# Optimization experiments

Measured on AMD Instinct MI355X. Metric: run time of the kernel, lower is better.

The kernel has to match this reference:

```python
import jax, jax.numpy as jnp
import numpy as np

N_NODES = 65536
N_EDGES = 524288
N_GRAPHS = 64
PTS_PER_GRAPH = 1024


def gcn_conv(x, W, b, row, col, self_idx, n_nodes):
    # PyG GCNConv: x' = D^{-1/2} (A + I) D^{-1/2} x W + b
    xw = x @ W
    row2 = jnp.concatenate([row, self_idx])
    col2 = jnp.concatenate([col, self_idx])
    deg = jax.ops.segment_sum(jnp.ones_like(col2, dtype=xw.dtype), col2, num_segments=n_nodes)
    dinv = jax.lax.rsqrt(deg)  # deg >= 1 thanks to self-loops
    norm = dinv[row2] * dinv[col2]  # [E+N]
    out = jax.ops.segment_sum(xw[row2] * norm[:, None], col2, num_segments=n_nodes)
    return out + b


def setup_inputs() -> dict:
    key = jax.random.key(0)
    ks = jax.random.split(key, 12)

    def glorot(k, fan_in, fan_out):
        s = jnp.sqrt(6.0 / (fan_in + fan_out))
        return jax.random.uniform(k, (fan_in, fan_out), jnp.float32, -s, s)

    x = jax.random.normal(ks[0], (N_NODES, 3), jnp.float32)
    edge_index = jax.random.randint(ks[1], (2, N_EDGES), 0, N_NODES, dtype=jnp.int64)
    batch = (jnp.arange(N_NODES, dtype=jnp.int64) // PTS_PER_GRAPH)  # 64 graphs x 1024 pts

    return {
        "x": x, "edge_index": edge_index, "batch": batch,
        "W1": glorot(ks[2], 3, 64), "b1": jnp.zeros((64,), jnp.float32),
        "W2": glorot(ks[3], 64, 256), "b2": jnp.zeros((256,), jnp.float32),
        "W3": glorot(ks[4], 256, 512), "b3": jnp.zeros((512,), jnp.float32),
        "Wm1": glorot(ks[5], 1024, 512), "bm1": jnp.zeros((512,), jnp.float32),
        "Wm2": glorot(ks[6], 512, 10), "bm2": jnp.zeros((10,), jnp.float32),
    }


def reference(x, edge_index, batch, W1, b1, W2, b2, W3, b3, Wm1, bm1, Wm2, bm2):
    n = x.shape[0]
    row, col = edge_index[0], edge_index[1]
    self_idx = jnp.arange(n, dtype=edge_index.dtype)

    x1 = jax.nn.relu(gcn_conv(x, W1, b1, row, col, self_idx, n))
    x2 = jax.nn.relu(gcn_conv(x1, W2, b2, row, col, self_idx, n))
    x3 = jax.nn.relu(gcn_conv(x2, W3, b3, row, col, self_idx, n))

    # global mean / max pool over batch segments
    counts = jax.ops.segment_sum(jnp.ones((n,), x3.dtype), batch, num_segments=N_GRAPHS)
    x_mean = jax.ops.segment_sum(x3, batch, num_segments=N_GRAPHS) / counts[:, None]
    x_max = jax.ops.segment_max(x3, batch, num_segments=N_GRAPHS)
    h = jnp.concatenate([x_mean, x_max], axis=1)  # [G, 1024]

    h = jax.nn.relu(h @ Wm1 + bm1)  # dropout is identity in eval
    return h @ Wm2 + bm2  # [G, 10]
```

## Files before the change

kernel.cpp:

```cpp
#include <hip/hip_runtime.h>
#include <hip/hip_bf16.h>

typedef __hip_bfloat16 bf16;
typedef short bf16x8 __attribute__((ext_vector_type(8)));
typedef float f32x4 __attribute__((ext_vector_type(4)));
typedef unsigned int u32x4 __attribute__((ext_vector_type(4)));

__device__ __forceinline__ float b2f_us(unsigned short u) {
    union { unsigned int i; float f; } c;
    c.i = ((unsigned int)u) << 16;
    return c.f;
}
__device__ __forceinline__ unsigned short f2b_us(float f) {
    bf16 h = __float2bfloat16(f);
    return *reinterpret_cast<unsigned short*>(&h);
}
__device__ __forceinline__ void unpack8(uint4 p, float* f) {
    f[0] = b2f_us(p.x & 0xffff); f[1] = b2f_us(p.x >> 16);
    f[2] = b2f_us(p.y & 0xffff); f[3] = b2f_us(p.y >> 16);
    f[4] = b2f_us(p.z & 0xffff); f[5] = b2f_us(p.z >> 16);
    f[6] = b2f_us(p.w & 0xffff); f[7] = b2f_us(p.w >> 16);
}

__device__ __forceinline__ void async_copy16(const bf16* g, bf16* l) {
    __builtin_amdgcn_global_load_lds(
        (const __attribute__((address_space(1))) unsigned int*)g,
        (__attribute__((address_space(3))) unsigned int*)l, 16, 0, 0);
}

__global__ __launch_bounds__(256) void k_count(const int* __restrict__ col,
                                               int* __restrict__ cnt,
                                               int* __restrict__ rank, int E) {
    int e = blockIdx.x * 256 + threadIdx.x;
    if (e < E) rank[e] = atomicAdd(cnt + col[e], 1);
}
__global__ __launch_bounds__(256) void k_scan_a(const int* __restrict__ cnt,
                                                int* __restrict__ bsum,
                                                float* __restrict__ dinv) {
    __shared__ int s[256];
    int t = threadIdx.x;
    int i = blockIdx.x * 256 + t;
    int c = cnt[i];
    dinv[i] = rsqrtf((float)c + 1.0f);
    s[t] = c;
    __syncthreads();
#pragma unroll
    for (int off = 128; off >= 1; off >>= 1) {
        if (t < off) s[t] += s[t + off];
        __syncthreads();
    }
    if (t == 0) bsum[blockIdx.x] = s[0];
}
__global__ __launch_bounds__(256) void k_scan_b(const int* __restrict__ bsum,
                                                int* __restrict__ boff) {
    __shared__ int s[256];
    int t = threadIdx.x;
    int self = bsum[t];
    s[t] = self;
    __syncthreads();
#pragma unroll
    for (int off = 1; off < 256; off <<= 1) {
        int v = (t >= off) ? s[t - off] : 0;
        __syncthreads();
        s[t] += v;
        __syncthreads();
    }
    boff[t] = s[t] - self;
}
__global__ __launch_bounds__(256) void k_scan_c(const int* __restrict__ cnt,
                                                const int* __restrict__ boff,
                                                int* __restrict__ rowptr) {
    __shared__ int s[256];
    int t = threadIdx.x;
    int base = blockIdx.x * 256;
    int self = cnt[base + t];
    s[t] = self;
    __syncthreads();
#pragma unroll
    for (int off = 1; off < 256; off <<= 1) {
        int v = (t >= off) ? s[t - off] : 0;
        __syncthreads();
        s[t] += v;
        __syncthreads();
    }
    rowptr[base + t] = boff[blockIdx.x] + s[t] - self;
}

__global__ __launch_bounds__(256) void k_scatter(const int* __restrict__ row,
                                                 const int* __restrict__ col,
                                                 const float* __restrict__ dinv,
                                                 const int* __restrict__ rowptr,
                                                 const int* __restrict__ rank,
                                                 int2* __restrict__ adj, int E) {
    int e = blockIdx.x * 256 + threadIdx.x;
    if (e >= E) return;
    int r = row[e], c = col[e];
    int pos = rowptr[c] + rank[e];
    adj[pos] = make_int2(r, __float_as_int(dinv[r]));
}

__global__ __launch_bounds__(256) void k_prep_all(const float* __restrict__ W2,
                                                  bf16* __restrict__ WT2,
                                                  const float* __restrict__ W3,
                                                  bf16* __restrict__ WT3) {
    int idx = blockIdx.x * 256 + threadIdx.x;
    if (idx < 64 * 256) {
        int k = idx >> 8, n = idx & 255;
        WT2[n * 64 + k] = __float2bfloat16(W2[idx]);
    } else {
        int i = idx - 64 * 256;
        if (i < 256 * 512) {
            int k = i >> 9, n = i & 511;
            WT3[(size_t)n * 256 + k] = __float2bfloat16(W3[i]);
        }
    }
}

__global__ __launch_bounds__(256) void k_gcn1(const int2* __restrict__ adj,
                                              const int* __restrict__ rowptr,
                                              const int* __restrict__ cnt,
                                              const float* __restrict__ dinv,
                                              const float* __restrict__ x,
                                              const float* __restrict__ W,
                                              const float* __restrict__ bias,
                                              bf16* __restrict__ h1, int N) {
    __shared__ float w[256];
    int t = threadIdx.x;
    if (t < 192) w[t] = W[t];
    else w[t] = bias[t - 192];
    __syncthreads();
    int n = blockIdx.x * 256 + t;
    if (n >= N) return;
    float d = dinv[n];
    float d2 = d * d;
    float a0 = x[n * 3] * d2, a1 = x[n * 3 + 1] * d2, a2 = x[n * 3 + 2] * d2;
    int beg = rowptr[n], end = beg + cnt[n];
    for (int e = beg; e < end; ++e) {
        int2 ad = adj[e];
        float wt = __int_as_float(ad.y) * d;
        a0 += x[ad.x * 3] * wt;
        a1 += x[ad.x * 3 + 1] * wt;
        a2 += x[ad.x * 3 + 2] * wt;
    }
    bf16* dst = h1 + (size_t)n * 64;
#pragma unroll
    for (int fb = 0; fb < 8; ++fb) {
        uint4 r;
        unsigned v[4];
#pragma unroll
        for (int p = 0; p < 4; ++p) {
            int f0 = fb * 8 + p * 2;
            float u0 = fmaxf(a0 * w[f0] + a1 * w[64 + f0] + a2 * w[128 + f0] + w[192 + f0], 0.f);
            int f1 = f0 + 1;
            float u1 = fmaxf(a0 * w[f1] + a1 * w[64 + f1] + a2 * w[128 + f1] + w[192 + f1], 0.f);
            v[p] = (unsigned)f2b_us(u0) | ((unsigned)f2b_us(u1) << 16);
        }
        r.x = v[0]; r.y = v[1]; r.z = v[2]; r.w = v[3];
        *reinterpret_cast<uint4*>(dst + fb * 8) = r;
    }
}

template <int F>
__global__ __launch_bounds__(256, 8) void k_gather_pre(const int2* __restrict__ adj,
                                                       const int* __restrict__ rowptr,
                                                       const int* __restrict__ cnt,
                                                       const float* __restrict__ dinv,
                                                       const bf16* __restrict__ h,
                                                       bf16* __restrict__ agg, int N) {
    constexpr int LPN = F / 8;
    constexpr int GRP = 2 * LPN;
    constexpr int NPB = 256 / GRP;
    int t = threadIdx.x;
    int node = blockIdx.x * NPB + t / GRP;
    if (node >= N) return;
    int gl = t % GRP;
    int fs = gl % LPN;
    int half = gl / LPN;
    int fbase = fs * 8;
    float d = dinv[node];
    size_t sbase = (size_t)node * F + fbase;
    float a[8] = {0.f, 0.f, 0.f, 0.f, 0.f, 0.f, 0.f, 0.f};
    if (half == 0) {
        uint4 sp = *reinterpret_cast<const uint4*>(h + sbase);
        unpack8(sp, a);
        float d2 = d * d;
#pragma unroll
        for (int i = 0; i < 8; i++) a[i] *= d2;
    }
    int beg = rowptr[node];
    int deg = cnt[node];
    int mid = beg + ((deg + 1) >> 1);
    int e   = half ? mid : beg;
    int end = half ? (beg + deg) : mid;
    for (; e + 3 < end; e += 4) {
        int2 ad[4];
        uint4 p[4];
#pragma unroll
        for (int u = 0; u < 4; ++u) ad[u] = adj[e + u];
#pragma unroll
        for (int u = 0; u < 4; ++u)
            p[u] = *reinterpret_cast<const uint4*>(h + (size_t)ad[u].x * F + fbase);
#pragma unroll
        for (int u = 0; u < 4; ++u) {
            float wt = __int_as_float(ad[u].y) * d;
            float f[8];
            unpack8(p[u], f);
#pragma unroll
            for (int i = 0; i < 8; i++) a[i] += f[i] * wt;
        }
    }
    for (; e < end; ++e) {
        int2 ad = adj[e];
        float wt = __int_as_float(ad.y) * d;
        uint4 p = *reinterpret_cast<const uint4*>(h + (size_t)ad.x * F + fbase);
        float f[8];
        unpack8(p, f);
#pragma unroll
        for (int i = 0; i < 8; i++) a[i] += f[i] * wt;
    }
#pragma unroll
    for (int i = 0; i < 8; i++) a[i] += __shfl_xor(a[i], LPN);
    if (half == 0) {
        u32x4 r;
        r.x = (unsigned)f2b_us(a[0]) | ((unsigned)f2b_us(a[1]) << 16);
        r.y = (unsigned)f2b_us(a[2]) | ((unsigned)f2b_us(a[3]) << 16);
        r.z = (unsigned)f2b_us(a[4]) | ((unsigned)f2b_us(a[5]) << 16);
        r.w = (unsigned)f2b_us(a[6]) | ((unsigned)f2b_us(a[7]) << 16);
        __builtin_nontemporal_store(r, reinterpret_cast<u32x4*>(agg + sbase));
    }
}

__global__ __launch_bounds__(256) void k_gemm_br(const bf16* __restrict__ A,
                                                 const bf16* __restrict__ BT,
                                                 const float* __restrict__ bias,
                                                 bf16* __restrict__ C,
                                                 int M, int N, int K) {
    __shared__ bf16 As[128 * 32];
    __shared__ bf16 Bs[128 * 32];
    const int t = threadIdx.x;
    const int wave = t >> 6, lane = t & 63;
    const int quad = lane >> 4, l16 = lane & 15;
    const int wm = wave & 1, wn = wave >> 1;
    const int m0 = blockIdx.x * 128;
    const int n0 = blockIdx.y * 128;

    f32x4 acc[4][4] = {};
    for (int kb = 0; kb < K; kb += 32) {
#pragma unroll
        for (int rnd = 0; rnd < 2; ++rnd) {
            int c = (rnd * 4 + wave) * 64 + lane;
            int r = c >> 2, seg = c & 3;
            async_copy16(A + (size_t)(m0 + r) * K + kb + seg * 8, As + c * 8);
            async_copy16(BT + (size_t)(n0 + r) * K + kb + seg * 8, Bs + c * 8);
        }
        __syncthreads();
        bf16x8 af[4], bfr[4];
#pragma unroll
        for (int i = 0; i < 4; i++)
            af[i] = *reinterpret_cast<const bf16x8*>(&As[(wm * 64 + i * 16 + l16) * 32 + quad * 8]);
#pragma unroll
        for (int j = 0; j < 4; j++)
            bfr[j] = *reinterpret_cast<const bf16x8*>(&Bs[(wn * 64 + j * 16 + l16) * 32 + quad * 8]);
#pragma unroll
        for (int i = 0; i < 4; i++)
#pragma unroll
            for (int j = 0; j < 4; j++)
                acc[i][j] = __builtin_amdgcn_mfma_f32_16x16x32_bf16(af[i], bfr[j], acc[i][j], 0, 0, 0);
        __syncthreads();
    }
#pragma unroll
    for (int j = 0; j < 4; j++) {
        int cn = n0 + wn * 64 + j * 16 + l16;
        float bv = bias[cn];
#pragma unroll
        for (int i = 0; i < 4; i++) {
            int row = m0 + wm * 64 + i * 16 + quad * 4;
#pragma unroll
            for (int r = 0; r < 4; r++)
                C[(size_t)(row + r) * N + cn] = __float2bfloat16(fmaxf(acc[i][j][r] + bv, 0.f));
        }
    }
}

__global__ __launch_bounds__(256) void k_gemm_pool(const bf16* __restrict__ A,
                                                   const bf16* __restrict__ BT,
                                                   const float* __restrict__ bias,
                                                   float* __restrict__ partials,
                                                   int M, int N, int K) {
    __shared__ bf16 As[128 * 32];
    __shared__ bf16 Bs[128 * 32];
    const int t = threadIdx.x;
    const int wave = t >> 6, lane = t & 63;
    const int quad = lane >> 4, l16 = lane & 15;
    const int wm = wave & 1, wn = wave >> 1;
    const int m0 = blockIdx.x * 128;
    const int n0 = blockIdx.y * 128;

    f32x4 acc[4][4] = {};
    for (int kb = 0; kb < K; kb += 32) {
#pragma unroll
        for (int rnd = 0; rnd < 2; ++rnd) {
            int c = (rnd * 4 + wave) * 64 + lane;
            int r = c >> 2, seg = c & 3;
            async_copy16(A + (size_t)(m0 + r) * K + kb + seg * 8, As + c * 8);
            async_copy16(BT + (size_t)(n0 + r) * K + kb + seg * 8, Bs + c * 8);
        }
        __syncthreads();
        bf16x8 af[4], bfr[4];
#pragma unroll
        for (int i = 0; i < 4; i++)
            af[i] = *reinterpret_cast<const bf16x8*>(&As[(wm * 64 + i * 16 + l16) * 32 + quad * 8]);
#pragma unroll
        for (int j = 0; j < 4; j++)
            bfr[j] = *reinterpret_cast<const bf16x8*>(&Bs[(wn * 64 + j * 16 + l16) * 32 + quad * 8]);
#pragma unroll
        for (int i = 0; i < 4; i++)
#pragma unroll
            for (int j = 0; j < 4; j++)
                acc[i][j] = __builtin_amdgcn_mfma_f32_16x16x32_bf16(af[i], bfr[j], acc[i][j], 0, 0, 0);
        __syncthreads();
    }
    size_t pbase = ((size_t)(blockIdx.x * 4 + blockIdx.y) * 2 + wm) * 256;
#pragma unroll
    for (int j = 0; j < 4; j++) {
        int f128 = wn * 64 + j * 16 + l16;
        float bv = bias[n0 + f128];
        float s = 0.f, mx = 0.f;
#pragma unroll
        for (int i = 0; i < 4; i++)
#pragma unroll
            for (int r = 0; r < 4; r++) {
                float v = fmaxf(acc[i][j][r] + bv, 0.f);
                s += v;
                mx = fmaxf(mx, v);
            }
        s += __shfl_xor(s, 16);
        s += __shfl_xor(s, 32);
        mx = fmaxf(mx, __shfl_xor(mx, 16));
        mx = fmaxf(mx, __shfl_xor(mx, 32));
        if (quad == 0) {
            partials[pbase + f128] = s;
            partials[pbase + 128 + f128] = mx;
        }
    }
}

__global__ __launch_bounds__(256) void k_pool_final(const float* __restrict__ partials,
                                                    float* __restrict__ pooled) {
    int idx = blockIdx.x * 256 + threadIdx.x;
    int g = idx >> 9, f = idx & 511;
    int by = f >> 7, f128 = f & 127;
    float S = 0.f, M = 0.f;
#pragma unroll
    for (int tile = 0; tile < 8; ++tile) {
        int bx = g * 8 + tile;
#pragma unroll
        for (int wm = 0; wm < 2; ++wm) {
            size_t pbase = ((size_t)(bx * 4 + by) * 2 + wm) * 256;
            S += partials[pbase + f128];
            M = fmaxf(M, partials[pbase + 128 + f128]);
        }
    }
    pooled[g * 1024 + f] = S * (1.0f / 1024.0f);
    pooled[g * 1024 + 512 + f] = M;
}

__global__ __launch_bounds__(256) void k_mlp1(const float* __restrict__ pooled,
                                              const float* __restrict__ Wm1,
                                              const float* __restrict__ bm1,
                                              float* __restrict__ o) {
    __shared__ float hg[1024];
    __shared__ float red[256];
    int g = blockIdx.x;
    int t = threadIdx.x;
    int f64 = t & 63, kq = t >> 6;
    int f = blockIdx.y * 64 + f64;
#pragma unroll
    for (int i = 0; i < 4; i++) hg[t + i * 256] = pooled[g * 1024 + t + i * 256];
    __syncthreads();
    float acc = 0.f;
    int k0 = kq * 256;
#pragma unroll 8
    for (int k = k0; k < k0 + 256; ++k)
        acc += hg[k] * Wm1[(size_t)k * 512 + f];
    red[t] = acc;
    __syncthreads();
    if (t < 64) {
        float total = red[t] + red[t + 64] + red[t + 128] + red[t + 192] + bm1[f];
        o[g * 512 + f] = fmaxf(total, 0.f);
    }
}

__global__ __launch_bounds__(512) void k_mlp2(const float* __restrict__ h,
                                              const float* __restrict__ Wm2,
                                              const float* __restrict__ bm2,
                                              float* __restrict__ out) {
    int g = blockIdx.x;
    int t = threadIdx.x;
    int j = t >> 5, lane32 = t & 31;
    float acc = 0.f;
    if (j < 10) {
        int k0 = lane32 * 16;
#pragma unroll
        for (int i = 0; i < 16; ++i)
            acc += h[g * 512 + k0 + i] * Wm2[(size_t)(k0 + i) * 10 + j];
    }
#pragma unroll
    for (int m = 16; m >= 1; m >>= 1) acc += __shfl_xor(acc, m);
    if (j < 10 && lane32 == 0) out[g * 10 + j] = acc + bm2[j];
}

extern "C" void kernel_launch(void* const* d_in, const int* in_sizes, int n_in,
                              void* d_out, int out_size, void* d_ws, size_t ws_size,
                              hipStream_t stream) {
    const float* x   = (const float*)d_in[0];
    const int*   ei  = (const int*)d_in[1];
    const float* W1  = (const float*)d_in[3];
    const float* b1  = (const float*)d_in[4];
    const float* W2  = (const float*)d_in[5];
    const float* b2  = (const float*)d_in[6];
    const float* W3  = (const float*)d_in[7];
    const float* b3  = (const float*)d_in[8];
    const float* Wm1 = (const float*)d_in[9];
    const float* bm1 = (const float*)d_in[10];
    const float* Wm2 = (const float*)d_in[11];
    const float* bm2 = (const float*)d_in[12];
    float* out = (float*)d_out;

    const int N = in_sizes[0] / 3;
    const int E = in_sizes[1] / 2;
    const int* row = ei;
    const int* col = ei + E;

    char* ws = (char*)d_ws;
    size_t off = 0;
    auto alloc = [&](size_t bytes) {
        void* p = ws + off;
        off += (bytes + 255) & ~(size_t)255;
        return p;
    };
    int*   cnt      = (int*)alloc((size_t)N * 4);
    int*   rowptr   = (int*)alloc((size_t)N * 4);
    float* dinv     = (float*)alloc((size_t)N * 4);
    int*   bsum     = (int*)alloc(256 * 4);
    int*   boff     = (int*)alloc(256 * 4);
    int*   rank     = (int*)alloc((size_t)E * 4);
    int2*  adj      = (int2*)alloc((size_t)E * 8);
    bf16*  h1       = (bf16*)alloc((size_t)N * 64 * 2);
    bf16*  agg2     = (bf16*)alloc((size_t)N * 64 * 2);
    bf16*  h2       = (bf16*)alloc((size_t)N * 256 * 2);
    bf16*  agg3     = (bf16*)alloc((size_t)N * 256 * 2);
    bf16*  WT2      = (bf16*)alloc(256 * 64 * 2);
    bf16*  WT3      = (bf16*)alloc(512 * 256 * 2);
    float* partials = (float*)alloc((size_t)512 * 4 * 2 * 256 * 4);
    float* pooled   = (float*)alloc(64 * 1024 * 4);
    float* m1       = (float*)alloc(64 * 512 * 4);

    (void)hipMemsetAsync(cnt, 0, (size_t)N * 4, stream);
    k_count<<<(E + 255) / 256, 256, 0, stream>>>(col, cnt, rank, E);
    k_scan_a<<<256, 256, 0, stream>>>(cnt, bsum, dinv);
    k_scan_b<<<1, 256, 0, stream>>>(bsum, boff);
    k_scan_c<<<256, 256, 0, stream>>>(cnt, boff, rowptr);
    k_scatter<<<(E + 255) / 256, 256, 0, stream>>>(row, col, dinv, rowptr, rank, adj, E);

    k_prep_all<<<(64 * 256 + 256 * 512 + 255) / 256, 256, 0, stream>>>(W2, WT2, W3, WT3);

    k_gcn1<<<(N + 255) / 256, 256, 0, stream>>>(adj, rowptr, cnt, dinv, x, W1, b1, h1, N);

    k_gather_pre<64><<<(N * 16) / 256, 256, 0, stream>>>(adj, rowptr, cnt, dinv, h1, agg2, N);
    k_gemm_br<<<dim3(N / 128, 256 / 128), 256, 0, stream>>>(agg2, WT2, b2, h2, N, 256, 64);

    k_gather_pre<256><<<(N * 64) / 256, 256, 0, stream>>>(adj, rowptr, cnt, dinv, h2, agg3, N);
    k_gemm_pool<<<dim3(N / 128, 512 / 128), 256, 0, stream>>>(agg3, WT3, b3, partials, N, 512, 256);
    k_pool_final<<<(64 * 512) / 256, 256, 0, stream>>>(partials, pooled);

    k_mlp1<<<dim3(64, 8), 256, 0, stream>>>(pooled, Wm1, bm1, m1);
    k_mlp2<<<64, 512, 0, stream>>>(m1, Wm2, bm2, out);
}
```

Before: 259.9 us.

## Fuse neighbor aggregation with MFMA GEMM for GCN layers 2 and 3

New measurement: 318.6 us. +22.6%, slower.

```diff
diff --git a/kernel.cpp b/kernel.cpp
--- a/kernel.cpp
+++ b/kernel.cpp
@@ -20,12 +20,6 @@
     f[2] = b2f_us(p.y & 0xffff); f[3] = b2f_us(p.y >> 16);
     f[4] = b2f_us(p.z & 0xffff); f[5] = b2f_us(p.z >> 16);
     f[6] = b2f_us(p.w & 0xffff); f[7] = b2f_us(p.w >> 16);
-}
-
-__device__ __forceinline__ void async_copy16(const bf16* g, bf16* l) {
-    __builtin_amdgcn_global_load_lds(
-        (const __attribute__((address_space(1))) unsigned int*)g,
-        (__attribute__((address_space(3))) unsigned int*)l, 16, 0, 0);
 }
 
 __global__ __launch_bounds__(256) void k_count(const int* __restrict__ col,
@@ -160,187 +154,239 @@
     }
 }
 
-template <int F>
-__global__ __launch_bounds__(256, 8) void k_gather_pre(const int2* __restrict__ adj,
-                                                       const int* __restrict__ rowptr,
-                                                       const int* __restrict__ cnt,
-                                                       const float* __restrict__ dinv,
-                                                       const bf16* __restrict__ h,
-                                                       bf16* __restrict__ agg, int N) {
-    constexpr int LPN = F / 8;
-    constexpr int GRP = 2 * LPN;
-    constexpr int NPB = 256 / GRP;
-    int t = threadIdx.x;
-    int node = blockIdx.x * NPB + t / GRP;
-    if (node >= N) return;
-    int gl = t % GRP;
-    int fs = gl % LPN;
-    int half = gl / LPN;
-    int fbase = fs * 8;
-    float d = dinv[node];
-    size_t sbase = (size_t)node * F + fbase;
-    float a[8] = {0.f, 0.f, 0.f, 0.f, 0.f, 0.f, 0.f, 0.f};
-    if (half == 0) {
-        uint4 sp = *reinterpret_cast<const uint4*>(h + sbase);
-        unpack8(sp, a);
-        float d2 = d * d;
-#pragma unroll
-        for (int i = 0; i < 8; i++) a[i] *= d2;
-    }
-    int beg = rowptr[node];
-    int deg = cnt[node];
-    int mid = beg + ((deg + 1) >> 1);
-    int e   = half ? mid : beg;
-    int end = half ? (beg + deg) : mid;
-    for (; e + 3 < end; e += 4) {
-        int2 ad[4];
-        uint4 p[4];
-#pragma unroll
-        for (int u = 0; u < 4; ++u) ad[u] = adj[e + u];
-#pragma unroll
-        for (int u = 0; u < 4; ++u)
-            p[u] = *reinterpret_cast<const uint4*>(h + (size_t)ad[u].x * F + fbase);
-#pragma unroll
-        for (int u = 0; u < 4; ++u) {
-            float wt = __int_as_float(ad[u].y) * d;
-            float f[8];
-            unpack8(p[u], f);
-#pragma unroll
-            for (int i = 0; i < 8; i++) a[i] += f[i] * wt;
-        }
-    }
-    for (; e < end; ++e) {
-        int2 ad = adj[e];
-        float wt = __int_as_float(ad.y) * d;
-        uint4 p = *reinterpret_cast<const uint4*>(h + (size_t)ad.x * F + fbase);
-        float f[8];
-        unpack8(p, f);
-#pragma unroll
-        for (int i = 0; i < 8; i++) a[i] += f[i] * wt;
-    }
-#pragma unroll
-    for (int i = 0; i < 8; i++) a[i] += __shfl_xor(a[i], LPN);
-    if (half == 0) {
-        u32x4 r;
-        r.x = (unsigned)f2b_us(a[0]) | ((unsigned)f2b_us(a[1]) << 16);
-        r.y = (unsigned)f2b_us(a[2]) | ((unsigned)f2b_us(a[3]) << 16);
-        r.z = (unsigned)f2b_us(a[4]) | ((unsigned)f2b_us(a[5]) << 16);
-        r.w = (unsigned)f2b_us(a[6]) | ((unsigned)f2b_us(a[7]) << 16);
-        __builtin_nontemporal_store(r, reinterpret_cast<u32x4*>(agg + sbase));
-    }
-}
-
-__global__ __launch_bounds__(256) void k_gemm_br(const bf16* __restrict__ A,
-                                                 const bf16* __restrict__ BT,
-                                                 const float* __restrict__ bias,
-                                                 bf16* __restrict__ C,
-                                                 int M, int N, int K) {
-    __shared__ bf16 As[128 * 32];
-    __shared__ bf16 Bs[128 * 32];
-    const int t = threadIdx.x;
-    const int wave = t >> 6, lane = t & 63;
-    const int quad = lane >> 4, l16 = lane & 15;
-    const int wm = wave & 1, wn = wave >> 1;
-    const int m0 = blockIdx.x * 128;
-    const int n0 = blockIdx.y * 128;
-
-    f32x4 acc[4][4] = {};
-    for (int kb = 0; kb < K; kb += 32) {
-#pragma unroll
-        for (int rnd = 0; rnd < 2; ++rnd) {
-            int c = (rnd * 4 + wave) * 64 + lane;
-            int r = c >> 2, seg = c & 3;
-            async_copy16(A + (size_t)(m0 + r) * K + kb + seg * 8, As + c * 8);
-            async_copy16(BT + (size_t)(n0 + r) * K + kb + seg * 8, Bs + c * 8);
-        }
-        __syncthreads();
-        bf16x8 af[4], bfr[4];
-#pragma unroll
-        for (int i = 0; i < 4; i++)
-            af[i] = *reinterpret_cast<const bf16x8*>(&As[(wm * 64 + i * 16 + l16) * 32 + quad * 8]);
-#pragma unroll
-        for (int j = 0; j < 4; j++)
-            bfr[j] = *reinterpret_cast<const bf16x8*>(&Bs[(wn * 64 + j * 16 + l16) * 32 + quad * 8]);
-#pragma unroll
-        for (int i = 0; i < 4; i++)
-#pragma unroll
-            for (int j = 0; j < 4; j++)
-                acc[i][j] = __builtin_amdgcn_mfma_f32_16x16x32_bf16(af[i], bfr[j], acc[i][j], 0, 0, 0);
-        __syncthreads();
-    }
-#pragma unroll
-    for (int j = 0; j < 4; j++) {
-        int cn = n0 + wn * 64 + j * 16 + l16;
-        float bv = bias[cn];
-#pragma unroll
-        for (int i = 0; i < 4; i++) {
-            int row = m0 + wm * 64 + i * 16 + quad * 4;
-#pragma unroll
-            for (int r = 0; r < 4; r++)
-                C[(size_t)(row + r) * N + cn] = __float2bfloat16(fmaxf(acc[i][j][r] + bv, 0.f));
-        }
-    }
-}
-
-__global__ __launch_bounds__(256) void k_gemm_pool(const bf16* __restrict__ A,
+__global__ __launch_bounds__(512, 4) void k_fused2(const int2* __restrict__ adj,
+                                                   const int* __restrict__ rowptr,
+                                                   const int* __restrict__ cnt,
+                                                   const float* __restrict__ dinv,
+                                                   const bf16* __restrict__ h,
                                                    const bf16* __restrict__ BT,
                                                    const float* __restrict__ bias,
-                                                   float* __restrict__ partials,
-                                                   int M, int N, int K) {
-    __shared__ bf16 As[128 * 32];
-    __shared__ bf16 Bs[128 * 32];
+                                                   bf16* __restrict__ C, int N) {
+    __shared__ bf16 As[128 * 64];
     const int t = threadIdx.x;
-    const int wave = t >> 6, lane = t & 63;
+    const int m0 = blockIdx.x * 128;
+    {
+        const int gi = t >> 4;
+        const int gl = t & 15;
+        const int half = gl >> 3, fs = gl & 7;
+        const int fbase = fs * 8;
+#pragma unroll 1
+        for (int p = 0; p < 4; ++p) {
+            int r = p * 32 + gi;
+            int node = m0 + r;
+            float d = dinv[node];
+            float a[8] = {0.f, 0.f, 0.f, 0.f, 0.f, 0.f, 0.f, 0.f};
+            if (half == 0) {
+                uint4 sp = *reinterpret_cast<const uint4*>(h + (size_t)node * 64 + fbase);
+                unpack8(sp, a);
+                float d2 = d * d;
+#pragma unroll
+                for (int i = 0; i < 8; i++) a[i] *= d2;
+            }
+            int beg = rowptr[node], deg = cnt[node];
+            int mid = beg + ((deg + 1) >> 1);
+            int e = half ? mid : beg;
+            int end = half ? (beg + deg) : mid;
+            for (; e + 3 < end; e += 4) {
+                int2 ad[4];
+                uint4 pl[4];
+#pragma unroll
+                for (int u = 0; u < 4; ++u) ad[u] = adj[e + u];
+#pragma unroll
+                for (int u = 0; u < 4; ++u)
+                    pl[u] = *reinterpret_cast<const uint4*>(h + (size_t)ad[u].x * 64 + fbase);
+#pragma unroll
+                for (int u = 0; u < 4; ++u) {
+                    float wt = __int_as_float(ad[u].y) * d;
+                    float f[8];
+                    unpack8(pl[u], f);
+#pragma unroll
+                    for (int i = 0; i < 8; i++) a[i] += f[i] * wt;
+                }
+            }
+            for (; e < end; ++e) {
+                int2 ad = adj[e];
+                float wt = __int_as_float(ad.y) * d;
+                uint4 pl = *reinterpret_cast<const uint4*>(h + (size_t)ad.x * 64 + fbase);
+                float f[8];
+                unpack8(pl, f);
+#pragma unroll
+                for (int i = 0; i < 8; i++) a[i] += f[i] * wt;
+            }
+#pragma unroll
+            for (int i = 0; i < 8; i++) a[i] += __shfl_xor(a[i], 8);
+            if (half == 0) {
+                u32x4 rr;
+                rr.x = (unsigned)f2b_us(a[0]) | ((unsigned)f2b_us(a[1]) << 16);
+                rr.y = (unsigned)f2b_us(a[2]) | ((unsigned)f2b_us(a[3]) << 16);
+                rr.z = (unsigned)f2b_us(a[4]) | ((unsigned)f2b_us(a[5]) << 16);
+                rr.w = (unsigned)f2b_us(a[6]) | ((unsigned)f2b_us(a[7]) << 16);
+                int c = fs ^ (r & 7);
+                *reinterpret_cast<u32x4*>(&As[r * 64 + c * 8]) = rr;
+            }
+        }
+    }
+    __syncthreads();
+    const int w = t >> 6, lane = t & 63;
     const int quad = lane >> 4, l16 = lane & 15;
-    const int wm = wave & 1, wn = wave >> 1;
+    const int wm = w & 1, wn = w >> 1;
+#pragma unroll 1
+    for (int nb = 0; nb < 2; ++nb) {
+        f32x4 acc[4][2] = {};
+#pragma unroll
+        for (int kb = 0; kb < 64; kb += 32) {
+            bf16x8 af[4], bfr[2];
+#pragma unroll
+            for (int i = 0; i < 4; i++) {
+                int R = wm * 64 + i * 16 + l16;
+                int c = ((kb >> 3) + quad) ^ (R & 7);
+                af[i] = *reinterpret_cast<const bf16x8*>(&As[R * 64 + c * 8]);
+            }
+#pragma unroll
+            for (int j = 0; j < 2; j++) {
+                int n = nb * 128 + wn * 32 + j * 16 + l16;
+                bfr[j] = *reinterpret_cast<const bf16x8*>(BT + (size_t)n * 64 + kb + quad * 8);
+            }
+#pragma unroll
+            for (int i = 0; i < 4; i++)
+#pragma unroll
+                for (int j = 0; j < 2; j++)
+                    acc[i][j] = __builtin_amdgcn_mfma_f32_16x16x32_bf16(af[i], bfr[j], acc[i][j], 0, 0, 0);
+        }
+#pragma unroll
+        for (int j = 0; j < 2; j++) {
+            int cn = nb * 128 + wn * 32 + j * 16 + l16;
+            float bv = bias[cn];
+#pragma unroll
+            for (int i = 0; i < 4; i++) {
+                int row = m0 + wm * 64 + i * 16 + quad * 4;
+#pragma unroll
+                for (int r = 0; r < 4; r++)
+                    C[(size_t)(row + r) * 256 + cn] = __float2bfloat16(fmaxf(acc[i][j][r] + bv, 0.f));
+            }
+        }
+    }
+}
+
+__global__ __launch_bounds__(512, 4) void k_fused3(const int2* __restrict__ adj,
+                                                   const int* __restrict__ rowptr,
+                                                   const int* __restrict__ cnt,
+                                                   const float* __restrict__ dinv,
+                                                   const bf16* __restrict__ h,
+                                                   const bf16* __restrict__ BT,
+                                                   const float* __restrict__ bias,
+                                                   float* __restrict__ partials, int N) {
+    __shared__ bf16 As[128 * 256];
+    const int t = threadIdx.x;
+    const int w = t >> 6, lane = t & 63;
     const int m0 = blockIdx.x * 128;
-    const int n0 = blockIdx.y * 128;
-
-    f32x4 acc[4][4] = {};
-    for (int kb = 0; kb < K; kb += 32) {
-#pragma unroll
-        for (int rnd = 0; rnd < 2; ++rnd) {
-            int c = (rnd * 4 + wave) * 64 + lane;
-            int r = c >> 2, seg = c & 3;
-            async_copy16(A + (size_t)(m0 + r) * K + kb + seg * 8, As + c * 8);
-            async_copy16(BT + (size_t)(n0 + r) * K + kb + seg * 8, Bs + c * 8);
-        }
-        __syncthreads();
-        bf16x8 af[4], bfr[4];
-#pragma unroll
-        for (int i = 0; i < 4; i++)
-            af[i] = *reinterpret_cast<const bf16x8*>(&As[(wm * 64 + i * 16 + l16) * 32 + quad * 8]);
-#pragma unroll
-        for (int j = 0; j < 4; j++)
-            bfr[j] = *reinterpret_cast<const bf16x8*>(&Bs[(wn * 64 + j * 16 + l16) * 32 + quad * 8]);
-#pragma unroll
-        for (int i = 0; i < 4; i++)
-#pragma unroll
-            for (int j = 0; j < 4; j++)
-                acc[i][j] = __builtin_amdgcn_mfma_f32_16x16x32_bf16(af[i], bfr[j], acc[i][j], 0, 0, 0);
-        __syncthreads();
-    }
-    size_t pbase = ((size_t)(blockIdx.x * 4 + blockIdx.y) * 2 + wm) * 256;
-#pragma unroll
-    for (int j = 0; j < 4; j++) {
-        int f128 = wn * 64 + j * 16 + l16;
-        float bv = bias[n0 + f128];
-        float s = 0.f, mx = 0.f;
-#pragma unroll
-        for (int i = 0; i < 4; i++)
-#pragma unroll
-            for (int r = 0; r < 4; r++) {
-                float v = fmaxf(acc[i][j][r] + bv, 0.f);
-                s += v;
-                mx = fmaxf(mx, v);
-            }
-        s += __shfl_xor(s, 16);
-        s += __shfl_xor(s, 32);
-        mx = fmaxf(mx, __shfl_xor(mx, 16));
-        mx = fmaxf(mx, __shfl_xor(mx, 32));
-        if (quad == 0) {
-            partials[pbase + f128] = s;
-            partials[pbase + 128 + f128] = mx;
+    {
+        const int half = lane >> 5, fs = lane & 31;
+        const int fbase = fs * 8;
+#pragma unroll 1
+        for (int p = 0; p < 16; ++p) {
+            int r = p * 8 + w;
+            int node = m0 + r;
+            float d = dinv[node];
+            float a[8] = {0.f, 0.f, 0.f, 0.f, 0.f, 0.f, 0.f, 0.f};
+            if (half == 0) {
+                uint4 sp = *reinterpret_cast<const uint4*>(h + (size_t)node * 256 + fbase);
+                unpack8(sp, a);
+                float d2 = d * d;
+#pragma unroll
+                for (int i = 0; i < 8; i++) a[i] *= d2;
+            }
+            int beg = rowptr[node], deg = cnt[node];
+            int mid = beg + ((deg + 1) >> 1);
+            int e = half ? mid : beg;
+            int end = half ? (beg + deg) : mid;
+            for (; e + 3 < end; e += 4) {
+                int2 ad[4];
+                uint4 pl[4];
+#pragma unroll
+                for (int u = 0; u < 4; ++u) ad[u] = adj[e + u];
+#pragma unroll
+                for (int u = 0; u < 4; ++u)
+                    pl[u] = *reinterpret_cast<const uint4*>(h + (size_t)ad[u].x * 256 + fbase);
+#pragma unroll
+                for (int u = 0; u < 4; ++u) {
+                    float wt = __int_as_float(ad[u].y) * d;
+                    float f[8];
+                    unpack8(pl[u], f);
+#pragma unroll
+                    for (int i = 0; i < 8; i++) a[i] += f[i] * wt;
+                }
+            }
+            for (; e < end; ++e) {
+                int2 ad = adj[e];
+                float wt = __int_as_float(ad.y) * d;
+                uint4 pl = *reinterpret_cast<const uint4*>(h + (size_t)ad.x * 256 + fbase);
+                float f[8];
+                unpack8(pl, f);
+#pragma unroll
+                for (int i = 0; i < 8; i++) a[i] += f[i] * wt;
+            }
+#pragma unroll
+            for (int i = 0; i < 8; i++) a[i] += __shfl_xor(a[i], 32);
+            if (half == 0) {
+                u32x4 rr;
+                rr.x = (unsigned)f2b_us(a[0]) | ((unsigned)f2b_us(a[1]) << 16);
+                rr.y = (unsigned)f2b_us(a[2]) | ((unsigned)f2b_us(a[3]) << 16);
+                rr.z = (unsigned)f2b_us(a[4]) | ((unsigned)f2b_us(a[5]) << 16);
+                rr.w = (unsigned)f2b_us(a[6]) | ((unsigned)f2b_us(a[7]) << 16);
+                int c = fs ^ (r & 7);
+                *reinterpret_cast<u32x4*>(&As[r * 256 + c * 8]) = rr;
+            }
+        }
+    }
+    __syncthreads();
+    const int quad = lane >> 4, l16 = lane & 15;
+    const int wm = w & 1, wn = w >> 1;
+#pragma unroll 1
+    for (int nb = 0; nb < 4; ++nb) {
+        f32x4 acc[4][2] = {};
+#pragma unroll
+        for (int kb = 0; kb < 256; kb += 32) {
+            bf16x8 af[4], bfr[2];
+#pragma unroll
+            for (int i = 0; i < 4; i++) {
+                int R = wm * 64 + i * 16 + l16;
+                int c = ((kb >> 3) + quad) ^ (R & 7);
+                af[i] = *reinterpret_cast<const bf16x8*>(&As[R * 256 + c * 8]);
+            }
+#pragma unroll
+            for (int j = 0; j < 2; j++) {
+                int n = nb * 128 + wn * 32 + j * 16 + l16;
+                bfr[j] = *reinterpret_cast<const bf16x8*>(BT + (size_t)n * 256 + kb + quad * 8);
+            }
+#pragma unroll
+            for (int i = 0; i < 4; i++)
+#pragma unroll
+                for (int j = 0; j < 2; j++)
+                    acc[i][j] = __builtin_amdgcn_mfma_f32_16x16x32_bf16(af[i], bfr[j], acc[i][j], 0, 0, 0);
+        }
+        size_t pbase = ((size_t)(blockIdx.x * 4 + nb) * 2 + wm) * 256;
+#pragma unroll
+        for (int j = 0; j < 2; j++) {
+            int f128 = wn * 32 + j * 16 + l16;
+            float bv = bias[nb * 128 + f128];
+            float s = 0.f, mx = 0.f;
+#pragma unroll
+            for (int i = 0; i < 4; i++)
+#pragma unroll
+                for (int r = 0; r < 4; r++) {
+                    float v = fmaxf(acc[i][j][r] + bv, 0.f);
+                    s += v;
+                    mx = fmaxf(mx, v);
+                }
+            s += __shfl_xor(s, 16);
+            s += __shfl_xor(s, 32);
+            mx = fmaxf(mx, __shfl_xor(mx, 16));
+            mx = fmaxf(mx, __shfl_xor(mx, 32));
+            if (quad == 0) {
+                partials[pbase + f128] = s;
+                partials[pbase + 128 + f128] = mx;
+            }
         }
     }
 }
@@ -447,9 +493,7 @@
     int*   rank     = (int*)alloc((size_t)E * 4);
     int2*  adj      = (int2*)alloc((size_t)E * 8);
     bf16*  h1       = (bf16*)alloc((size_t)N * 64 * 2);
-    bf16*  agg2     = (bf16*)alloc((size_t)N * 64 * 2);
     bf16*  h2       = (bf16*)alloc((size_t)N * 256 * 2);
-    bf16*  agg3     = (bf16*)alloc((size_t)N * 256 * 2);
     bf16*  WT2      = (bf16*)alloc(256 * 64 * 2);
     bf16*  WT3      = (bf16*)alloc(512 * 256 * 2);
     float* partials = (float*)alloc((size_t)512 * 4 * 2 * 256 * 4);
@@ -467,11 +511,9 @@
 
     k_gcn1<<<(N + 255) / 256, 256, 0, stream>>>(adj, rowptr, cnt, dinv, x, W1, b1, h1, N);
 
-    k_gather_pre<64><<<(N * 16) / 256, 256, 0, stream>>>(adj, rowptr, cnt, dinv, h1, agg2, N);
-    k_gemm_br<<<dim3(N / 128, 256 / 128), 256, 0, stream>>>(agg2, WT2, b2, h2, N, 256, 64);
-
-    k_gather_pre<256><<<(N * 64) / 256, 256, 0, stream>>>(adj, rowptr, cnt, dinv, h2, agg3, N);
-    k_gemm_pool<<<dim3(N / 128, 512 / 128), 256, 0, stream>>>(agg3, WT3, b3, partials, N, 512, 256);
+    k_fused2<<<N / 128, 512, 0, stream>>>(adj, rowptr, cnt, dinv, h1, WT2, b2, h2, N);
+
+    k_fused3<<<N / 128, 512, 0, stream>>>(adj, rowptr, cnt, dinv, h2, WT3, b3, partials, N);
     k_pool_final<<<(64 * 512) / 256, 256, 0, stream>>>(partials, pooled);
 
     k_mlp1<<<dim3(64, 8), 256, 0, stream>>>(pooled, Wm1, bm1, m1);
```

## Stage full A row-block in LDS once and loop over N tiles

Applied to the files above, without the earlier changes.

Measured after the change: 322.0 us. 1.24x slower.

```diff
diff --git a/kernel.cpp b/kernel.cpp
--- a/kernel.cpp
+++ b/kernel.cpp
@@ -230,117 +230,125 @@
     }
 }
 
-__global__ __launch_bounds__(256) void k_gemm_br(const bf16* __restrict__ A,
-                                                 const bf16* __restrict__ BT,
-                                                 const float* __restrict__ bias,
-                                                 bf16* __restrict__ C,
-                                                 int M, int N, int K) {
-    __shared__ bf16 As[128 * 32];
-    __shared__ bf16 Bs[128 * 32];
+__global__ __launch_bounds__(512, 4) void k_gemm2(const bf16* __restrict__ A,
+                                                  const bf16* __restrict__ BT,
+                                                  const float* __restrict__ bias,
+                                                  bf16* __restrict__ C) {
+    __shared__ bf16 As[128 * 64];
     const int t = threadIdx.x;
-    const int wave = t >> 6, lane = t & 63;
+    const int m0 = blockIdx.x * 128;
+#pragma unroll
+    for (int i = 0; i < 2; ++i) {
+        int c = i * 512 + t;
+        int r = c >> 3, q = c & 7;
+        int qs = q ^ (r & 7);
+        async_copy16(A + (size_t)(m0 + r) * 64 + qs * 8, As + c * 8);
+    }
+    __syncthreads();
+    const int w = t >> 6, lane = t & 63;
     const int quad = lane >> 4, l16 = lane & 15;
-    const int wm = wave & 1, wn = wave >> 1;
+    const int wm = w & 1, wn = w >> 1;
+#pragma unroll 1
+    for (int nb = 0; nb < 2; ++nb) {
+        f32x4 acc[4][2] = {};
+#pragma unroll
+        for (int kb = 0; kb < 64; kb += 32) {
+            bf16x8 af[4], bfr[2];
+#pragma unroll
+            for (int i = 0; i < 4; i++) {
+                int R = wm * 64 + i * 16 + l16;
+                int q = ((kb >> 3) + quad) ^ (R & 7);
+                af[i] = *reinterpret_cast<const bf16x8*>(&As[R * 64 + q * 8]);
+            }
+#pragma unroll
+            for (int j = 0; j < 2; j++) {
+                int n = nb * 128 + wn * 32 + j * 16 + l16;
+                bfr[j] = *reinterpret_cast<const bf16x8*>(BT + (size_t)n * 64 + kb + quad * 8);
+            }
+#pragma unroll
+            for (int i = 0; i < 4; i++)
+#pragma unroll
+                for (int j = 0; j < 2; j++)
+                    acc[i][j] = __builtin_amdgcn_mfma_f32_16x16x32_bf16(af[i], bfr[j], acc[i][j], 0, 0, 0);
+        }
+#pragma unroll
+        for (int j = 0; j < 2; j++) {
+            int cn = nb * 128 + wn * 32 + j * 16 + l16;
+            float bv = bias[cn];
+#pragma unroll
+            for (int i = 0; i < 4; i++) {
+                int row = m0 + wm * 64 + i * 16 + quad * 4;
+#pragma unroll
+                for (int r = 0; r < 4; r++)
+                    C[(size_t)(row + r) * 256 + cn] = __float2bfloat16(fmaxf(acc[i][j][r] + bv, 0.f));
+            }
+        }
+    }
+}
+
+__global__ __launch_bounds__(512, 4) void k_gemm3(const bf16* __restrict__ A,
+                                                  const bf16* __restrict__ BT,
+                                                  const float* __restrict__ bias,
+                                                  float* __restrict__ partials) {
+    __shared__ bf16 As[128 * 256];
+    const int t = threadIdx.x;
     const int m0 = blockIdx.x * 128;
-    const int n0 = blockIdx.y * 128;
-
-    f32x4 acc[4][4] = {};
-    for (int kb = 0; kb < K; kb += 32) {
-#pragma unroll
-        for (int rnd = 0; rnd < 2; ++rnd) {
-            int c = (rnd * 4 + wave) * 64 + lane;
-            int r = c >> 2, seg = c & 3;
-            async_copy16(A + (size_t)(m0 + r) * K + kb + seg * 8, As + c * 8);
-            async_copy16(BT + (size_t)(n0 + r) * K + kb + seg * 8, Bs + c * 8);
-        }
-        __syncthreads();
-        bf16x8 af[4], bfr[4];
-#pragma unroll
-        for (int i = 0; i < 4; i++)
-            af[i] = *reinterpret_cast<const bf16x8*>(&As[(wm * 64 + i * 16 + l16) * 32 + quad * 8]);
-#pragma unroll
-        for (int j = 0; j < 4; j++)
-            bfr[j] = *reinterpret_cast<const bf16x8*>(&Bs[(wn * 64 + j * 16 + l16) * 32 + quad * 8]);
-#pragma unroll
-        for (int i = 0; i < 4; i++)
-#pragma unroll
-            for (int j = 0; j < 4; j++)
-                acc[i][j] = __builtin_amdgcn_mfma_f32_16x16x32_bf16(af[i], bfr[j], acc[i][j], 0, 0, 0);
-        __syncthreads();
-    }
-#pragma unroll
-    for (int j = 0; j < 4; j++) {
-        int cn = n0 + wn * 64 + j * 16 + l16;
-        float bv = bias[cn];
-#pragma unroll
-        for (int i = 0; i < 4; i++) {
-            int row = m0 + wm * 64 + i * 16 + quad * 4;
-#pragma unroll
-            for (int r = 0; r < 4; r++)
-                C[(size_t)(row + r) * N + cn] = __float2bfloat16(fmaxf(acc[i][j][r] + bv, 0.f));
-        }
-    }
-}
-
-__global__ __launch_bounds__(256) void k_gemm_pool(const bf16* __restrict__ A,
-                                                   const bf16* __restrict__ BT,
-                                                   const float* __restrict__ bias,
-                                                   float* __restrict__ partials,
-                                                   int M, int N, int K) {
-    __shared__ bf16 As[128 * 32];
-    __shared__ bf16 Bs[128 * 32];
-    const int t = threadIdx.x;
-    const int wave = t >> 6, lane = t & 63;
+#pragma unroll
+    for (int i = 0; i < 8; ++i) {
+        int c = i * 512 + t;
+        int r = c >> 5, q = c & 31;
+        int qs = q ^ (r & 7);
+        async_copy16(A + (size_t)(m0 + r) * 256 + qs * 8, As + c * 8);
+    }
+    __syncthreads();
+    const int w = t >> 6, lane = t & 63;
     const int quad = lane >> 4, l16 = lane & 15;
-    const int wm = wave & 1, wn = wave >> 1;
-    const int m0 = blockIdx.x * 128;
-    const int n0 = blockIdx.y * 128;
-
-    f32x4 acc[4][4] = {};
-    for (int kb = 0; kb < K; kb += 32) {
-#pragma unroll
-        for (int rnd = 0; rnd < 2; ++rnd) {
-            int c = (rnd * 4 + wave) * 64 + lane;
-            int r = c >> 2, seg = c & 3;
-            async_copy16(A + (size_t)(m0 + r) * K + kb + seg * 8, As + c * 8);
-            async_copy16(BT + (size_t)(n0 + r) * K + kb + seg * 8, Bs + c * 8);
-        }
-        __syncthreads();
-        bf16x8 af[4], bfr[4];
-#pragma unroll
-        for (int i = 0; i < 4; i++)
-            af[i] = *reinterpret_cast<const bf16x8*>(&As[(wm * 64 + i * 16 + l16) * 32 + quad * 8]);
-#pragma unroll
-        for (int j = 0; j < 4; j++)
-            bfr[j] = *reinterpret_cast<const bf16x8*>(&Bs[(wn * 64 + j * 16 + l16) * 32 + quad * 8]);
-#pragma unroll
-        for (int i = 0; i < 4; i++)
-#pragma unroll
-            for (int j = 0; j < 4; j++)
-                acc[i][j] = __builtin_amdgcn_mfma_f32_16x16x32_bf16(af[i], bfr[j], acc[i][j], 0, 0, 0);
-        __syncthreads();
-    }
-    size_t pbase = ((size_t)(blockIdx.x * 4 + blockIdx.y) * 2 + wm) * 256;
-#pragma unroll
-    for (int j = 0; j < 4; j++) {
-        int f128 = wn * 64 + j * 16 + l16;
-        float bv = bias[n0 + f128];
-        float s = 0.f, mx = 0.f;
-#pragma unroll
-        for (int i = 0; i < 4; i++)
-#pragma unroll
-            for (int r = 0; r < 4; r++) {
-                float v = fmaxf(acc[i][j][r] + bv, 0.f);
-                s += v;
-                mx = fmaxf(mx, v);
-            }
-        s += __shfl_xor(s, 16);
-        s += __shfl_xor(s, 32);
-        mx = fmaxf(mx, __shfl_xor(mx, 16));
-        mx = fmaxf(mx, __shfl_xor(mx, 32));
-        if (quad == 0) {
-            partials[pbase + f128] = s;
-            partials[pbase + 128 + f128] = mx;
+    const int wm = w & 1, wn = w >> 1;
+#pragma unroll 1
+    for (int nb = 0; nb < 4; ++nb) {
+        f32x4 acc[4][2] = {};
+#pragma unroll
+        for (int kb = 0; kb < 256; kb += 32) {
+            bf16x8 af[4], bfr[2];
+#pragma unroll
+            for (int i = 0; i < 4; i++) {
+                int R = wm * 64 + i * 16 + l16;
+                int q = ((kb >> 3) + quad) ^ (R & 7);
+                af[i] = *reinterpret_cast<const bf16x8*>(&As[R * 256 + q * 8]);
+            }
+#pragma unroll
+            for (int j = 0; j < 2; j++) {
+                int n = nb * 128 + wn * 32 + j * 16 + l16;
+                bfr[j] = *reinterpret_cast<const bf16x8*>(BT + (size_t)n * 256 + kb + quad * 8);
+            }
+#pragma unroll
+            for (int i = 0; i < 4; i++)
+#pragma unroll
+                for (int j = 0; j < 2; j++)
+                    acc[i][j] = __builtin_amdgcn_mfma_f32_16x16x32_bf16(af[i], bfr[j], acc[i][j], 0, 0, 0);
+        }
+        size_t pbase = ((size_t)(blockIdx.x * 4 + nb) * 2 + wm) * 256;
+#pragma unroll
+        for (int j = 0; j < 2; j++) {
+            int f128 = wn * 32 + j * 16 + l16;
+            float bv = bias[nb * 128 + f128];
+            float s = 0.f, mx = 0.f;
+#pragma unroll
+            for (int i = 0; i < 4; i++)
+#pragma unroll
+                for (int r = 0; r < 4; r++) {
+                    float v = fmaxf(acc[i][j][r] + bv, 0.f);
+                    s += v;
+                    mx = fmaxf(mx, v);
+                }
+            s += __shfl_xor(s, 16);
+            s += __shfl_xor(s, 32);
+            mx = fmaxf(mx, __shfl_xor(mx, 16));
+            mx = fmaxf(mx, __shfl_xor(mx, 32));
+            if (quad == 0) {
+                partials[pbase + f128] = s;
+                partials[pbase + 128 + f128] = mx;
+            }
         }
     }
 }
@@ -468,10 +476,10 @@
     k_gcn1<<<(N + 255) / 256, 256, 0, stream>>>(adj, rowptr, cnt, dinv, x, W1, b1, h1, N);
 
     k_gather_pre<64><<<(N * 16) / 256, 256, 0, stream>>>(adj, rowptr, cnt, dinv, h1, agg2, N);
-    k_gemm_br<<<dim3(N / 128, 256 / 128), 256, 0, stream>>>(agg2, WT2, b2, h2, N, 256, 64);
+    k_gemm2<<<N / 128, 512, 0, stream>>>(agg2, WT2, b2, h2);
 
     k_gather_pre<256><<<(N * 64) / 256, 256, 0, stream>>>(adj, rowptr, cnt, dinv, h2, agg3, N);
-    k_gemm_pool<<<dim3(N / 128, 512 / 128), 256, 0, stream>>>(agg3, WT3, b3, partials, N, 512, 256);
+    k_gemm3<<<N / 128, 512, 0, stream>>>(agg3, WT3, b3, partials);
     k_pool_final<<<(64 * 512) / 256, 256, 0, stream>>>(partials, pooled);
 
     k_mlp1<<<dim3(64, 8), 256, 0, stream>>>(pooled, Wm1, bm1, m1);
```
